# Kernel optimization log

Measured on AMD Instinct MI355X. Metric: run time of the kernel, lower is better.

The kernel has to match this reference:

```python
import jax, jax.numpy as jnp
import numpy as np

IN_F = 256
OUT_F = 256
HOP = 3
ALPHA = 0.2   # LeakyReLU negative slope
BETA = 0.5    # hop mixing coefficient
N = 50000
E = 1600000


def setup_inputs() -> dict:
    key = jax.random.key(0)
    k1, k2, k3, k4 = jax.random.split(key, 4)
    inp = jax.random.normal(k1, (N, IN_F), dtype=jnp.float32)
    k_edge_list = jax.random.randint(k2, (HOP, 2, E), 0, N, dtype=jnp.int32)
    # xavier_normal-ish scales
    W = jax.random.normal(k3, (IN_F * HOP, OUT_F), dtype=jnp.float32) * (1.414 * np.sqrt(2.0 / (IN_F * HOP + OUT_F)))
    a = jax.random.normal(k4, (1, 2 * OUT_F * HOP), dtype=jnp.float32) * (1.414 * np.sqrt(2.0 / (1 + 2 * OUT_F * HOP)))
    return {"input": inp, "k_edge_list": k_edge_list, "W": W, "a": a}


def reference(input, k_edge_list, W, a):
    n = input.shape[0]
    h_prime_return = jnp.zeros((n, OUT_F), dtype=input.dtype)
    for i in range(HOP - 1, -1, -1):
        # per-hop projection: h = input @ W[i*in : (i+1)*in]  -> [N, OUT_F]
        h = input @ W[i * IN_F:(i + 1) * IN_F, :]
        src = k_edge_list[i, 0]  # [E] row indices (scatter targets)
        dst = k_edge_list[i, 1]  # [E] col indices (gather sources)
        ai = a[0, 2 * i * OUT_F:(2 * i + 2) * OUT_F]
        # a_i . cat(h[src], h[dst]) == (h @ a_src)[src] + (h @ a_dst)[dst]
        s_src = h @ ai[:OUT_F]   # [N]
        s_dst = h @ ai[OUT_F:]   # [N]
        score = s_src[src] + s_dst[dst]                     # [E]
        edge_e = jnp.exp(-jax.nn.leaky_relu(score, ALPHA))  # [E]
        # sparse row-sum: spmm(A, ones)
        e_rowsum = jax.ops.segment_sum(edge_e, src, num_segments=n)          # [N]
        # weighted aggregate: spmm(A, h)
        h_prime = jax.ops.segment_sum(edge_e[:, None] * h[dst], src, num_segments=n)  # [N, OUT_F]
        h_prime = h_prime / e_rowsum[:, None]
        h_prime_return = (1.0 - BETA) * h_prime + BETA * h_prime_return
    return jax.nn.elu(h_prime_return)  # concat=True path
```

## Files before the change

### kernel.cpp

```cpp
#include <hip/hip_runtime.h>

#define N_NODES 50000
#define E_EDGES 1600000
#define HOPS    3
#define KDIM    256
#define NOUT    768
#define MPAD    50048
#define NPS     50176
#define NCB     196
#define NCB_ALL (NCB * HOPS)
#define HSTRIDE ((size_t)MPAD * 256)
#define PCAP    10240
#define RCAP    9216
#define SEB     4096

typedef unsigned short u16;
typedef __bf16 bf16x8 __attribute__((ext_vector_type(8)));
typedef float  f32x4  __attribute__((ext_vector_type(4)));

__device__ __forceinline__ u16 f2bf(float f) {
  unsigned u = __float_as_uint(f);
  u += 0x7fffu + ((u >> 16) & 1u);
  return (u16)(u >> 16);
}
__device__ __forceinline__ float bf2f(u16 h) {
  return __uint_as_float(((unsigned)h) << 16);
}

__device__ __forceinline__ void gl2lds16(const void* g, void* l) {
  __builtin_amdgcn_global_load_lds(
      (__attribute__((address_space(1))) void*)(g),
      (__attribute__((address_space(3))) void*)(l), 16, 0, 0);
}

__global__ __launch_bounds__(256) void conv_a(const float* __restrict__ in,
                                              u16* __restrict__ A) {
  int idx  = blockIdx.x * 256 + threadIdx.x;
  int base = idx * 4;
  int row  = base >> 8;
  ushort4 o;
  if (row < N_NODES) {
    float4 v = *(const float4*)(in + base);
    o.x = f2bf(v.x); o.y = f2bf(v.y); o.z = f2bf(v.z); o.w = f2bf(v.w);
  } else {
    o.x = 0; o.y = 0; o.z = 0; o.w = 0;
  }
  *(ushort4*)(A + base) = o;
}

__global__ __launch_bounds__(256) void conv_w(const float* __restrict__ W,
                                              u16* __restrict__ Bt) {
  __shared__ float tile[32][33];
  int h  = blockIdx.z;
  int c0 = blockIdx.x * 32;
  int k0 = blockIdx.y * 32;
  int x  = threadIdx.x & 31;
  int y0 = threadIdx.x >> 5;
#pragma unroll
  for (int i = 0; i < 4; ++i) {
    int k = k0 + y0 + i * 8;
    tile[y0 + i * 8][x] = W[(size_t)(h * 256 + k) * 256 + (c0 + x)];
  }
  __syncthreads();
#pragma unroll
  for (int i = 0; i < 4; ++i) {
    int c = c0 + y0 + i * 8;
    Bt[(size_t)(h * 256 + c) * 256 + (k0 + x)] = f2bf(tile[x][y0 + i * 8]);
  }
}

__global__ __launch_bounds__(256) void gemm_kernel(const u16* __restrict__ A,
                                                   const u16* __restrict__ B,
                                                   u16* __restrict__ H,
                                                   const float* __restrict__ a,
                                                   float* __restrict__ ssrc,
                                                   float* __restrict__ sdst) {
  __shared__ char lds[32768];
  int tid  = threadIdx.x;
  int lane = tid & 63;
  int w    = tid >> 6;
  int wm   = w >> 1, wn = w & 1;
  int r    = lane & 15, q = lane >> 4;
  int bm   = blockIdx.y * 128, bn = blockIdx.x * 128;

  const u16* Ag0 = A + (size_t)(bm + 2 * w * 16 + r) * KDIM + q * 8;
  const u16* Bg0 = B + (size_t)(bn + 2 * w * 16 + r) * KDIM + q * 8;

  f32x4 zero = {0.f, 0.f, 0.f, 0.f};
  f32x4 acc[4][4];
#pragma unroll
  for (int mt = 0; mt < 4; ++mt)
#pragma unroll
    for (int nt = 0; nt < 4; ++nt) acc[mt][nt] = zero;

#define STAGE(b, kt)                                                      \
  do {                                                                    \
    int ko = (kt) * 32;                                                   \
    char* As_ = lds + (b) * 16384;                                        \
    char* Bs_ = As_ + 8192;                                               \
    gl2lds16(Ag0 + ko,             As_ + (2 * w) * 1024);                 \
    gl2lds16(Ag0 + 16 * KDIM + ko, As_ + (2 * w + 1) * 1024);             \
    gl2lds16(Bg0 + ko,             Bs_ + (2 * w) * 1024);                 \
    gl2lds16(Bg0 + 16 * KDIM + ko, Bs_ + (2 * w + 1) * 1024);             \
  } while (0)

  STAGE(0, 0);
  __syncthreads();

  for (int kt = 0; kt < 8; ++kt) {
    int cur = kt & 1;
    if (kt < 7) STAGE(cur ^ 1, kt + 1);
    char* As = lds + cur * 16384;
    char* Bs = As + 8192;
    bf16x8 af[4], bfv[4];
#pragma unroll
    for (int mt = 0; mt < 4; ++mt)
      af[mt] = *(const bf16x8*)(As + (wm * 4 + mt) * 1024 + lane * 16);
#pragma unroll
    for (int nt = 0; nt < 4; ++nt)
      bfv[nt] = *(const bf16x8*)(Bs + (wn * 4 + nt) * 1024 + lane * 16);
#pragma unroll
    for (int mt = 0; mt < 4; ++mt)
#pragma unroll
      for (int nt = 0; nt < 4; ++nt)
        acc[mt][nt] = __builtin_amdgcn_mfma_f32_16x16x32_bf16(
            af[mt], bfv[nt], acc[mt][nt], 0, 0, 0);
    if (kt < 7) __syncthreads();
  }
#undef STAGE

  int hop = bn >> 8;
  int cbase = (bn & 255) + wn * 64 + r;
  float asv[4], adv[4];
#pragma unroll
  for (int nt = 0; nt < 4; ++nt) {
    asv[nt] = a[hop * 512 + cbase + nt * 16];
    adv[nt] = a[hop * 512 + 256 + cbase + nt * 16];
  }
#pragma unroll
  for (int mt = 0; mt < 4; ++mt)
#pragma unroll
    for (int rg = 0; rg < 4; ++rg) {
      float ps = 0.f, pd = 0.f;
#pragma unroll
      for (int nt = 0; nt < 4; ++nt) {
        float v = acc[mt][nt][rg];
        ps += v * asv[nt];
        pd += v * adv[nt];
      }
#pragma unroll
      for (int m = 1; m < 16; m <<= 1) {
        ps += __shfl_xor(ps, m);
        pd += __shfl_xor(pd, m);
      }
      if (r == 0) {
        int row = bm + wm * 64 + mt * 16 + q * 4 + rg;
        if (row < N_NODES) {
          atomicAdd(&ssrc[hop * NPS + row], ps);
          atomicAdd(&sdst[hop * NPS + row], pd);
        }
      }
    }

#pragma unroll
  for (int mt = 0; mt < 4; ++mt)
#pragma unroll
    for (int nt = 0; nt < 4; ++nt)
#pragma unroll
      for (int rg = 0; rg < 4; ++rg) {
        int row = bm + wm * 64 + mt * 16 + q * 4 + rg;
        int col = bn + wn * 64 + nt * 16 + r;
        int c = col & 255;
        H[hop * HSTRIDE + (size_t)row * 256 + c] = f2bf(acc[mt][nt][rg]);
      }
}

__global__ __launch_bounds__(256) void init_ccur(int* __restrict__ ccur) {
  int t = blockIdx.x * 256 + threadIdx.x;
  if (t < NCB_ALL) ccur[t] = t * PCAP;
}

__global__ __launch_bounds__(256) void split1_kernel(const int* __restrict__ kel,
                                                     const float* __restrict__ ssrc,
                                                     const float* __restrict__ sdst,
                                                     int* __restrict__ ccur,
                                                     int2* __restrict__ packed) {
  __shared__ int2 stage[SEB];
  __shared__ int h[NCB];
  __shared__ int lofs[NCB];
  __shared__ int bbase[NCB];
  __shared__ int lcur[NCB];
  int t = threadIdx.x, hop = blockIdx.y;
  for (int i = t; i < NCB; i += 256) { h[i] = 0; lcur[i] = 0; }
  __syncthreads();
  const int* srcp = kel + (size_t)hop * 2 * E_EDGES;
  const int* dstp = srcp + E_EDGES;
  int e0 = blockIdx.x * SEB;
  int total = E_EDGES - e0; if (total > SEB) total = SEB;
  int esrc[16], edst[16];
#pragma unroll
  for (int i = 0; i < 16; ++i) {
    int e = e0 + i * 256 + t;
    if (e < E_EDGES) {
      esrc[i] = srcp[e];
      edst[i] = dstp[e];
      atomicAdd(&h[esrc[i] >> 8], 1);
    } else {
      esrc[i] = -1;
    }
  }
  __syncthreads();
  for (int i = t; i < NCB; i += 256)
    if (h[i]) bbase[i] = atomicAdd(&ccur[hop * NCB + i], h[i]);
  if (t < 64) {
    int run = 0;
#pragma unroll
    for (int c = 0; c < 4; ++c) {
      int idx = c * 64 + t;
      int v = (idx < NCB) ? h[idx] : 0;
      int s = v;
#pragma unroll
      for (int d = 1; d < 64; d <<= 1) {
        int x = __shfl_up(s, d);
        if (t >= d) s += x;
      }
      if (idx < NCB) lofs[idx] = run + s - v;
      run += __shfl(s, 63);
    }
  }
  __syncthreads();
#pragma unroll
  for (int i = 0; i < 16; ++i) {
    if (esrc[i] < 0) continue;
    int src = esrc[i], dst = edst[i];
    float s = ssrc[hop * NPS + src] + sdst[hop * NPS + dst];
    float lr = s > 0.0f ? s : 0.2f * s;
    float ee = __expf(-lr);
    int bin = src >> 8;
    int rank = atomicAdd(&lcur[bin], 1);
    stage[lofs[bin] + rank] =
        make_int2((bin << 24) | ((src & 255) << 16) | dst, __float_as_int(ee));
  }
  __syncthreads();
  for (int i = t; i < total; i += 256) {
    int2 r = stage[i];
    int bin = (unsigned)r.x >> 24;
    int pos = bbase[bin] + (i - lofs[bin]);
    packed[pos] = make_int2(r.x & 0x00FFFFFF, r.y);
  }
}

__global__ __launch_bounds__(1024) void fine_kernel(const int* __restrict__ ccur,
                                                    int2* __restrict__ packed,
                                                    int* __restrict__ offs,
                                                    int* __restrict__ counts) {
  __shared__ int h2[256];
  __shared__ int lc[256];
  __shared__ int wtot[4], wbase[4];
  int t = threadIdx.x;
  int b = blockIdx.x;
  int hop = b / NCB, bl = b % NCB;
  int base = b * PCAP;
  int cnt = ccur[b] - base;
  if (cnt > RCAP) cnt = RCAP;
  if (t < 256) h2[t] = 0;
  __syncthreads();
  int2 r0, r1, r2, r3, r4, r5, r6, r7, r8;
#define FLOAD(k, rv)                                                     \
  do {                                                                   \
    int idx = (k) * 1024 + t;                                            \
    if (idx < cnt) {                                                     \
      rv = packed[base + idx];                                           \
      atomicAdd(&h2[(rv.x >> 16) & 255], 1);                             \
    }                                                                    \
  } while (0)
  FLOAD(0, r0); FLOAD(1, r1); FLOAD(2, r2); FLOAD(3, r3); FLOAD(4, r4);
  FLOAD(5, r5); FLOAD(6, r6); FLOAD(7, r7); FLOAD(8, r8);
#undef FLOAD
  __syncthreads();
  int v = 0, s = 0;
  if (t < 256) {
    int lane = t & 63;
    v = h2[t];
    s = v;
#pragma unroll
    for (int d = 1; d < 64; d <<= 1) {
      int x = __shfl_up(s, d);
      if (lane >= d) s += x;
    }
    if (lane == 63) wtot[t >> 6] = s;
  }
  __syncthreads();
  if (t == 0) {
    int r = 0;
#pragma unroll
    for (int i = 0; i < 4; ++i) { wbase[i] = r; r += wtot[i]; }
  }
  __syncthreads();
  if (t < 256) {
    int ex = wbase[t >> 6] + s - v;
    int node = hop * NPS + bl * 256 + t;
    offs[node] = base + ex;
    counts[node] = v;
    lc[t] = ex;
  }
  __syncthreads();
#define FSCAT(k, rv)                                                     \
  do {                                                                   \
    int idx = (k) * 1024 + t;                                            \
    if (idx < cnt) {                                                     \
      int low = (rv.x >> 16) & 255;                                      \
      int rank = atomicAdd(&lc[low], 1);                                 \
      packed[base + rank] = make_int2(rv.x & 0xFFFF, rv.y);              \
    }                                                                    \
  } while (0)
  FSCAT(0, r0); FSCAT(1, r1); FSCAT(2, r2); FSCAT(3, r3); FSCAT(4, r4);
  FSCAT(5, r5); FSCAT(6, r6); FSCAT(7, r7); FSCAT(8, r8);
#undef FSCAT
}

__device__ __forceinline__ void accum8(float* a, float& rs, float ee, uint4 h) {
  rs += ee;
  a[0] += ee * __uint_as_float(h.x << 16);
  a[1] += ee * __uint_as_float(h.x & 0xffff0000u);
  a[2] += ee * __uint_as_float(h.y << 16);
  a[3] += ee * __uint_as_float(h.y & 0xffff0000u);
  a[4] += ee * __uint_as_float(h.z << 16);
  a[5] += ee * __uint_as_float(h.z & 0xffff0000u);
  a[6] += ee * __uint_as_float(h.w << 16);
  a[7] += ee * __uint_as_float(h.w & 0xffff0000u);
}

__global__ __launch_bounds__(256) void agg_all(const int* __restrict__ offs,
                                               const int* __restrict__ counts,
                                               const int2* __restrict__ packed,
                                               const u16* __restrict__ Hbf,
                                               float* __restrict__ out,
                                               int n0, int n1) {
  int lane = threadIdx.x & 63, wid = threadIdx.x >> 6;
  int half = lane >> 5, sub = lane & 31;
  int n = n0 + blockIdx.x * 4 + wid;
  if (n >= n1) return;

  float r[8];
#pragma unroll
  for (int c = 0; c < 8; ++c) r[c] = 0.f;

#pragma unroll
  for (int hop = 0; hop < HOPS; ++hop) {
    const float wgt = hop == 0 ? 0.5f : (hop == 1 ? 0.25f : 0.125f);
    int start = offs[hop * NPS + n];
    int cnt = counts[hop * NPS + n];
    const int2* pk = packed + start;
    const u16* Hh = Hbf + hop * HSTRIDE + sub * 8;
    float a0[8], a1[8];
    float rs0 = 0.f, rs1 = 0.f;
#pragma unroll
    for (int c = 0; c < 8; ++c) { a0[c] = 0.f; a1[c] = 0.f; }

    int np = cnt >> 1;
    int j = 0;
    for (; j + 8 <= np; j += 8) {
      int2 p[8];
#pragma unroll
      for (int i = 0; i < 8; ++i) p[i] = pk[2 * (j + i) + half];
      uint4 h[8];
#pragma unroll
      for (int i = 0; i < 8; ++i) h[i] = *(const uint4*)(Hh + (size_t)p[i].x * 256);
#pragma unroll
      for (int i = 0; i < 8; ++i)
        accum8((i & 1) ? a1 : a0, (i & 1) ? rs1 : rs0, __int_as_float(p[i].y), h[i]);
    }
    for (; j < np; ++j) {
      int2 p = pk[2 * j + half];
      uint4 hv = *(const uint4*)(Hh + (size_t)p.x * 256);
      accum8(a0, rs0, __int_as_float(p.y), hv);
    }
    if (cnt & 1) {
      int2 p = pk[cnt - 1];
      float ee = half ? 0.f : __int_as_float(p.y);
      uint4 hv = *(const uint4*)(Hh + (size_t)p.x * 256);
      accum8(a1, rs1, ee, hv);
    }

    float rs = rs0 + rs1;
    rs += __shfl_xor(rs, 32);
    float inv = wgt / rs;
#pragma unroll
    for (int c = 0; c < 8; ++c) {
      float t = a0[c] + a1[c];
      t += __shfl_xor(t, 32);
      r[c] += t * inv;
    }
  }

  float* op = out + (size_t)n * 256 + sub * 8 + half * 4;
  float4 o;
  float v0 = r[half * 4 + 0], v1 = r[half * 4 + 1];
  float v2 = r[half * 4 + 2], v3 = r[half * 4 + 3];
  o.x = v0 > 0.f ? v0 : expm1f(v0);
  o.y = v1 > 0.f ? v1 : expm1f(v1);
  o.z = v2 > 0.f ? v2 : expm1f(v2);
  o.w = v3 > 0.f ? v3 : expm1f(v3);
  *(float4*)op = o;
}

extern "C" void kernel_launch(void* const* d_in, const int* in_sizes, int n_in,
                              void* d_out, int out_size, void* d_ws, size_t ws_size,
                              hipStream_t stream) {
  const float* input = (const float*)d_in[0];
  const int*   kel   = (const int*)d_in[1];
  const float* W     = (const float*)d_in[2];
  const float* a     = (const float*)d_in[3];
  float* out = (float*)d_out;

  char* ws = (char*)d_ws;
  size_t o = 0;
  u16* Abf = (u16*)(ws + o);   o += (size_t)MPAD * KDIM * 2;
  u16* Bt  = (u16*)(ws + o);   o += (size_t)NOUT * KDIM * 2;
  u16* Hbf = (u16*)(ws + o);   o += (size_t)MPAD * NOUT * 2;
  float* ssrc = (float*)(ws + o); o += (size_t)3 * NPS * 4;
  float* sdst = (float*)(ws + o); o += (size_t)3 * NPS * 4;
  int* counts = (int*)(ws + o);   o += (size_t)3 * NPS * 4;
  int* offs   = (int*)(ws + o);   o += (size_t)3 * NPS * 4;
  int* ccur   = (int*)(ws + o);   o += 4096;
  int2* packed = (int2*)(ws + o); o += (size_t)NCB_ALL * PCAP * 8 + 65536;

  hipMemsetAsync(ssrc, 0, (size_t)2 * 3 * NPS * 4, stream);

  conv_a<<<MPAD * KDIM / 1024, 256, 0, stream>>>(input, Abf);
  conv_w<<<dim3(8, 8, 3), 256, 0, stream>>>(W, Bt);
  init_ccur<<<3, 256, 0, stream>>>(ccur);
  gemm_kernel<<<dim3(NOUT / 128, MPAD / 128), 256, 0, stream>>>(Abf, Bt, Hbf,
                                                                a, ssrc, sdst);

  int nsplit = (E_EDGES + SEB - 1) / SEB;
  split1_kernel<<<dim3(nsplit, 3), 256, 0, stream>>>(kel, ssrc, sdst, ccur, packed);
  fine_kernel<<<NCB_ALL, 1024, 0, stream>>>(ccur, packed, offs, counts);

  agg_all<<<2500, 256, 0, stream>>>(offs, counts, packed, Hbf, out, 0, 10000);
  agg_all<<<2500, 256, 0, stream>>>(offs, counts, packed, Hbf, out, 10000, 20000);
  agg_all<<<2500, 256, 0, stream>>>(offs, counts, packed, Hbf, out, 20000, 30000);
  agg_all<<<2500, 256, 0, stream>>>(offs, counts, packed, Hbf, out, 30000, 40000);
  agg_all<<<2500, 256, 0, stream>>>(offs, counts, packed, Hbf, out, 40000, 50000);
}
```

Measured before the change: 671.5 us.

## Scatter edges directly to global bins and merge aggregation launches

The split kernel no longer sorts edges by bin in shared memory before a contiguous copy-out. Each edge now claims a slot with a shared-memory atomic on the per-bin global base and writes straight to the packed array. This drops the LDS staging, the prefix scan and one barrier, at the cost of scattered, uncoalesced global writes. Separately, the five chunked aggregation launches are merged into a single launch over all nodes, removing launch overhead and tail gaps.

```diff
diff --git a/kernel.cpp b/kernel.cpp
--- a/kernel.cpp
+++ b/kernel.cpp
@@ -185,18 +185,14 @@
                                                      const float* __restrict__ sdst,
                                                      int* __restrict__ ccur,
                                                      int2* __restrict__ packed) {
-  __shared__ int2 stage[SEB];
   __shared__ int h[NCB];
-  __shared__ int lofs[NCB];
-  __shared__ int bbase[NCB];
   __shared__ int lcur[NCB];
   int t = threadIdx.x, hop = blockIdx.y;
-  for (int i = t; i < NCB; i += 256) { h[i] = 0; lcur[i] = 0; }
+  for (int i = t; i < NCB; i += 256) h[i] = 0;
   __syncthreads();
   const int* srcp = kel + (size_t)hop * 2 * E_EDGES;
   const int* dstp = srcp + E_EDGES;
   int e0 = blockIdx.x * SEB;
-  int total = E_EDGES - e0; if (total > SEB) total = SEB;
   int esrc[16], edst[16];
 #pragma unroll
   for (int i = 0; i < 16; ++i) {
@@ -211,23 +207,7 @@
   }
   __syncthreads();
   for (int i = t; i < NCB; i += 256)
-    if (h[i]) bbase[i] = atomicAdd(&ccur[hop * NCB + i], h[i]);
-  if (t < 64) {
-    int run = 0;
-#pragma unroll
-    for (int c = 0; c < 4; ++c) {
-      int idx = c * 64 + t;
-      int v = (idx < NCB) ? h[idx] : 0;
-      int s = v;
-#pragma unroll
-      for (int d = 1; d < 64; d <<= 1) {
-        int x = __shfl_up(s, d);
-        if (t >= d) s += x;
-      }
-      if (idx < NCB) lofs[idx] = run + s - v;
-      run += __shfl(s, 63);
-    }
-  }
+    if (h[i]) lcur[i] = atomicAdd(&ccur[hop * NCB + i], h[i]);
   __syncthreads();
 #pragma unroll
   for (int i = 0; i < 16; ++i) {
@@ -236,17 +216,8 @@
     float s = ssrc[hop * NPS + src] + sdst[hop * NPS + dst];
     float lr = s > 0.0f ? s : 0.2f * s;
     float ee = __expf(-lr);
-    int bin = src >> 8;
-    int rank = atomicAdd(&lcur[bin], 1);
-    stage[lofs[bin] + rank] =
-        make_int2((bin << 24) | ((src & 255) << 16) | dst, __float_as_int(ee));
-  }
-  __syncthreads();
-  for (int i = t; i < total; i += 256) {
-    int2 r = stage[i];
-    int bin = (unsigned)r.x >> 24;
-    int pos = bbase[bin] + (i - lofs[bin]);
-    packed[pos] = make_int2(r.x & 0x00FFFFFF, r.y);
+    int pos = atomicAdd(&lcur[src >> 8], 1);
+    packed[pos] = make_int2(((src & 255) << 16) | dst, __float_as_int(ee));
   }
 }
 
@@ -335,12 +306,11 @@
                                                const int* __restrict__ counts,
                                                const int2* __restrict__ packed,
                                                const u16* __restrict__ Hbf,
-                                               float* __restrict__ out,
-                                               int n0, int n1) {
+                                               float* __restrict__ out) {
   int lane = threadIdx.x & 63, wid = threadIdx.x >> 6;
   int half = lane >> 5, sub = lane & 31;
-  int n = n0 + blockIdx.x * 4 + wid;
-  if (n >= n1) return;
+  int n = blockIdx.x * 4 + wid;
+  if (n >= N_NODES) return;
 
   float r[8];
 #pragma unroll
@@ -438,9 +408,5 @@
   split1_kernel<<<dim3(nsplit, 3), 256, 0, stream>>>(kel, ssrc, sdst, ccur, packed);
   fine_kernel<<<NCB_ALL, 1024, 0, stream>>>(ccur, packed, offs, counts);
 
-  agg_all<<<2500, 256, 0, stream>>>(offs, counts, packed, Hbf, out, 0, 10000);
-  agg_all<<<2500, 256, 0, stream>>>(offs, counts, packed, Hbf, out, 10000, 20000);
-  agg_all<<<2500, 256, 0, stream>>>(offs, counts, packed, Hbf, out, 20000, 30000);
-  agg_all<<<2500, 256, 0, stream>>>(offs, counts, packed, Hbf, out, 30000, 40000);
-  agg_all<<<2500, 256, 0, stream>>>(offs, counts, packed, Hbf, out, 40000, 50000);
-}
+  agg_all<<<N_NODES / 4 + 1, 256, 0, stream>>>(offs, counts, packed, Hbf, out);
+}
```

After: 633.6 us. -5.6%, faster.
